# Kernel optimization log

Hardware: AMD Instinct MI355X
Metric: run time of the kernel (lower is better)

## Reference

```python
import jax, jax.numpy as jnp
import numpy as np

N = 100000   # nodes
E = 1000000  # edges
D = 128      # in_dim == out_dim (residual enabled)
EPS = 1e-5   # BatchNorm1d default eps


def setup_inputs() -> dict:
    key = jax.random.key(0)
    k = jax.random.split(key, 5)
    feature = jax.random.normal(k[0], (N, D), dtype=jnp.float32)
    src = jax.random.randint(k[1], (E,), 0, N, dtype=jnp.int32)
    dst = jax.random.randint(k[2], (E,), 0, N, dtype=jnp.int32)
    # nn.Linear(in_dim, out_dim): W is [out, in]
    W = jax.random.normal(k[3], (D, D), dtype=jnp.float32) / np.sqrt(D).astype(np.float32)
    b = jnp.zeros((D,), dtype=jnp.float32)
    gamma = jnp.ones((D,), dtype=jnp.float32)
    beta = jnp.zeros((D,), dtype=jnp.float32)
    return {"feature": feature, "src": src, "dst": dst, "W": W, "b": b,
            "gamma": gamma, "beta": beta}


def reference(feature, src, dst, W, b, gamma, beta):
    # update_all(copy_src('h'), mean): gather src features, mean-reduce onto dst
    deg = jax.ops.segment_sum(jnp.ones((E,), dtype=feature.dtype), dst,
                              num_segments=N)                      # [N]
    agg = jax.ops.segment_sum(feature[src], dst, num_segments=N)   # [N, D]
    agg = agg / jnp.maximum(deg, 1.0)[:, None]  # zero in-degree -> 0 (DGL mean)
    # NodeApplyModule: linear
    h = agg @ W.T + b                                              # [N, D]
    # BatchNorm1d over node dimension (training-mode batch stats, biased var)
    mean = jnp.mean(h, axis=0)
    var = jnp.var(h, axis=0)
    h = (h - mean) * jax.lax.rsqrt(var + EPS) * gamma + beta
    # activation, residual; dropout p=0.0 -> identity
    h = jax.nn.relu(h)
    h = feature + h
    return h
```

## Files before the change

kernel.cpp:

```cpp
#include <hip/hip_runtime.h>

typedef unsigned short u16;
typedef unsigned int u32;

#define D_DIM 128
#define CHUNK 4096
#define SCHUNK 4096
#define NPART 8

typedef __attribute__((ext_vector_type(8))) short bf16x8;
typedef __attribute__((ext_vector_type(4))) float f32x4;

__device__ __forceinline__ float bf2f(u16 h) {
    u32 u = ((u32)h) << 16;
    return __uint_as_float(u);
}
__device__ __forceinline__ u16 f2bf(float f) {
    u32 u = __float_as_uint(f);
    u32 r = (u >> 16) & 1u;
    u += 0x7fffu + r;
    return (u16)(u >> 16);
}
__device__ __forceinline__ float lo16(u32 u) { return bf2f((u16)(u & 0xffffu)); }
__device__ __forceinline__ float hi16(u32 u) { return bf2f((u16)(u >> 16)); }

__global__ void GCNLayer_76647986365164_kernel(int* p, int nwords,
                                               const u32* w, int* flag) {
    int i = blockIdx.x * blockDim.x + threadIdx.x;
    if (i < nwords) p[i] = 0;
    if (blockIdx.x == 0) {
        __shared__ int cnt;
        if (threadIdx.x == 0) cnt = 0;
        __syncthreads();
        int c = 0;
        for (int j = 0; j < 4; ++j) {
            u32 x = w[threadIdx.x * 4 + j];
            u32 e = (x >> 7) & 0xFFu;
            if (e >= 100u && e <= 140u) c++;
        }
        atomicAdd(&cnt, c);
        __syncthreads();
        if (threadIdx.x == 0) flag[0] = (cnt >= 700) ? 1 : 0;
    }
}

__global__ void k_deg(const int* __restrict__ dst, int* __restrict__ deg,
                      int* __restrict__ rank, int E) {
    int i = blockIdx.x * blockDim.x + threadIdx.x;
    if (i < E) rank[i] = atomicAdd(&deg[dst[i]], 1);
}

__global__ void k_scan_local(const int* deg, int* offs, int* bsums, int n) {
    __shared__ int tsum[256];
    const int tid = threadIdx.x;
    const int base = blockIdx.x * CHUNK + tid * 16;
    int v[16];
    int run = 0;
    for (int j = 0; j < 16; ++j) {
        int idx = base + j;
        v[j] = (idx < n) ? deg[idx] : 0;
        run += v[j];
    }
    tsum[tid] = run;
    __syncthreads();
    for (int off = 1; off < 256; off <<= 1) {
        int val = tsum[tid];
        int add = (tid >= off) ? tsum[tid - off] : 0;
        __syncthreads();
        tsum[tid] = val + add;
        __syncthreads();
    }
    int acc = tsum[tid] - run;
    for (int j = 0; j < 16; ++j) {
        int idx = base + j;
        if (idx < n) offs[idx] = acc;
        acc += v[j];
    }
    if (tid == 255) bsums[blockIdx.x] = tsum[255];
}

__global__ void k_scan_add(int* offs, const int* bsums, int n, int nblk) {
    __shared__ int carry_s;
    const int tid = threadIdx.x;
    const int b = blockIdx.x;
    if (tid == 0) {
        int c = 0;
        for (int i = 0; i < b; ++i) c += bsums[i];
        carry_s = c;
        if (b == nblk - 1) offs[n] = c + bsums[b];
    }
    __syncthreads();
    const int carry = carry_s;
    const int base = b * CHUNK + tid * 16;
    for (int j = 0; j < 16; ++j) {
        int idx = base + j;
        if (idx < n) offs[idx] += carry;
    }
}

__global__ void k_scatter(const int* __restrict__ src, const int* __restrict__ dst,
                          const int* __restrict__ rank, const int* __restrict__ offs,
                          int* __restrict__ csr, int E, int nper) {
    const int pr = blockIdx.x & (NPART - 1);
    const int s  = blockIdx.x >> 3;
    const int lo = pr * nper;
    const int hi = lo + nper;
    const int base = s * SCHUNK;
    int end = base + SCHUNK;
    if (end > E) end = E;
    for (int i = base + (int)threadIdx.x; i < end; i += 256) {
        int d = dst[i];
        if (d >= lo && d < hi) {
            csr[offs[d] + rank[i]] = src[i];
        }
    }
}

__global__ void k_aggregate(const void* feature, const int* offs,
                            const int* csr, u16* agg, const int* flag,
                            int n, int npad) {
    int node = blockIdx.x * 4 + (threadIdx.x >> 6);
    int lane = threadIdx.x & 63;
    if (node >= npad) return;
    const int g = lane >> 4;
    const int c = lane & 15;
    int bf = flag[0];
    float acc[8];
    #pragma unroll
    for (int t = 0; t < 8; ++t) acc[t] = 0.f;
    int degn = 0;
    if (node < n) {
        int s = offs[node], e = offs[node + 1];
        degn = e - s;
        if (bf) {
            const uint4* fq = (const uint4*)feature;
            for (int j = s; j < e; j += 16) {
                int j0 = j + g, j1 = j0 + 4, j2 = j0 + 8, j3 = j0 + 12;
                uint4 u0 = {0,0,0,0}, u1 = {0,0,0,0}, u2 = {0,0,0,0}, u3 = {0,0,0,0};
                if (j0 < e) u0 = fq[(size_t)csr[j0] * 16 + c];
                if (j1 < e) u1 = fq[(size_t)csr[j1] * 16 + c];
                if (j2 < e) u2 = fq[(size_t)csr[j2] * 16 + c];
                if (j3 < e) u3 = fq[(size_t)csr[j3] * 16 + c];
                #define ACC8(U) \
                    acc[0] += lo16(U.x); acc[1] += hi16(U.x); \
                    acc[2] += lo16(U.y); acc[3] += hi16(U.y); \
                    acc[4] += lo16(U.z); acc[5] += hi16(U.z); \
                    acc[6] += lo16(U.w); acc[7] += hi16(U.w);
                ACC8(u0); ACC8(u1); ACC8(u2); ACC8(u3);
                #undef ACC8
            }
        } else {
            const float4* fq = (const float4*)feature;
            for (int j = s; j < e; j += 8) {
                int j0 = j + g, j1 = j0 + 4;
                if (j0 < e) {
                    size_t b0 = (size_t)csr[j0] * 32 + c * 2;
                    float4 x = fq[b0], y = fq[b0 + 1];
                    acc[0] += x.x; acc[1] += x.y; acc[2] += x.z; acc[3] += x.w;
                    acc[4] += y.x; acc[5] += y.y; acc[6] += y.z; acc[7] += y.w;
                }
                if (j1 < e) {
                    size_t b1 = (size_t)csr[j1] * 32 + c * 2;
                    float4 x = fq[b1], y = fq[b1 + 1];
                    acc[0] += x.x; acc[1] += x.y; acc[2] += x.z; acc[3] += x.w;
                    acc[4] += y.x; acc[5] += y.y; acc[6] += y.z; acc[7] += y.w;
                }
            }
        }
    }
    #pragma unroll
    for (int t = 0; t < 8; ++t) {
        acc[t] += __shfl_xor(acc[t], 16);
        acc[t] += __shfl_xor(acc[t], 32);
    }
    float sc = 1.0f / (float)(degn > 1 ? degn : 1);
    if (g == 0) {
        uint4 o4;
        o4.x = (u32)f2bf(acc[0] * sc) | ((u32)f2bf(acc[1] * sc) << 16);
        o4.y = (u32)f2bf(acc[2] * sc) | ((u32)f2bf(acc[3] * sc) << 16);
        o4.z = (u32)f2bf(acc[4] * sc) | ((u32)f2bf(acc[5] * sc) << 16);
        o4.w = (u32)f2bf(acc[6] * sc) | ((u32)f2bf(acc[7] * sc) << 16);
        ((uint4*)(agg + (size_t)node * D_DIM))[c] = o4;
    }
}

__global__ void k_gemm(u16* agg, const void* W, const void* bias,
                       float* colsum, float* colsq, const int* flag, int n) {
    __shared__ u16 sW[128 * 136];
    __shared__ float bsum[128], bsq[128];
    const int tid = threadIdx.x;
    const int rb = blockIdx.x * 64;
    const int bf = flag[0];
    const int w = tid >> 6;
    const int lane = tid & 63;
    const int g = lane >> 4, c = lane & 15;

    if (tid < 128) { bsum[tid] = 0.f; bsq[tid] = 0.f; }

    bf16x8 afr[4];
    {
        const u16* arow = agg + (size_t)(rb + w * 16 + c) * D_DIM + g * 8;
        #pragma unroll
        for (int kt = 0; kt < 4; ++kt)
            afr[kt] = *(const bf16x8*)(arow + kt * 32);
    }

    f32x4 acc[8];
    #pragma unroll
    for (int ot = 0; ot < 8; ++ot) acc[ot] = (f32x4){0.f, 0.f, 0.f, 0.f};

    const int npass = bf ? 1 : 2;
    for (int pass = 0; pass < npass; ++pass) {
        if (bf) {
            #pragma unroll
            for (int i = 0; i < 8; ++i) {
                int e = (i * 256 + tid) * 8;
                int row = e >> 7, k = e & 127;
                *(uint4*)(&sW[row * 136 + k]) = *(const uint4*)((const u16*)W + e);
            }
        } else {
            const float* Wf = (const float*)W;
            #pragma unroll
            for (int i = 0; i < 8; ++i) {
                int e = (i * 256 + tid) * 8;
                int row = e >> 7, k = e & 127;
                float4 x = *(const float4*)(Wf + e);
                float4 y = *(const float4*)(Wf + e + 4);
                float v[8] = {x.x, x.y, x.z, x.w, y.x, y.y, y.z, y.w};
                u16 hb[8];
                #pragma unroll
                for (int j = 0; j < 8; ++j) {
                    u16 h = f2bf(v[j]);
                    if (pass == 1) h = f2bf(v[j] - bf2f(h));
                    hb[j] = h;
                }
                uint4 pk;
                pk.x = (u32)hb[0] | ((u32)hb[1] << 16);
                pk.y = (u32)hb[2] | ((u32)hb[3] << 16);
                pk.z = (u32)hb[4] | ((u32)hb[5] << 16);
                pk.w = (u32)hb[6] | ((u32)hb[7] << 16);
                *(uint4*)(&sW[row * 136 + k]) = pk;
            }
        }
        __syncthreads();
        #pragma unroll
        for (int ot = 0; ot < 8; ++ot) {
            const u16* wrow = &sW[(ot * 16 + c) * 136 + g * 8];
            #pragma unroll
            for (int kt = 0; kt < 4; ++kt) {
                bf16x8 bfr = *(const bf16x8*)(wrow + kt * 32);
                acc[ot] = __builtin_amdgcn_mfma_f32_16x16x32_bf16(
                    afr[kt], bfr, acc[ot], 0, 0, 0);
            }
        }
        if (pass + 1 < npass) __syncthreads();
    }

    const int rowbase = rb + w * 16 + g * 4;
    #pragma unroll
    for (int ot = 0; ot < 8; ++ot) {
        const int o = ot * 16 + c;
        float bv = bf ? bf2f(((const u16*)bias)[o]) : ((const float*)bias)[o];
        float s = 0.f, q = 0.f;
        float hv[4];
        #pragma unroll
        for (int r = 0; r < 4; ++r) {
            float h = acc[ot][r] + bv;
            hv[r] = h;
            if (rowbase + r < n) { s += h; q += h * h; }
        }
        #pragma unroll
        for (int r = 0; r < 4; ++r) {
            float hp = __shfl_xor(hv[r], 1);
            if (!(lane & 1)) {
                u32 pk = (u32)f2bf(hv[r]) | ((u32)f2bf(hp) << 16);
                *(u32*)(agg + (size_t)(rowbase + r) * D_DIM + o) = pk;
            }
        }
        s += __shfl_xor(s, 16); s += __shfl_xor(s, 32);
        q += __shfl_xor(q, 16); q += __shfl_xor(q, 32);
        if (g == 0) { atomicAdd(&bsum[o], s); atomicAdd(&bsq[o], q); }
    }
    __syncthreads();
    if (tid < 128) {
        atomicAdd(&colsum[tid], bsum[tid]);
        atomicAdd(&colsq[tid], bsq[tid]);
    }
}

__global__ void k_apply(const u16* h, const void* feature, const float* stats,
                        const void* gamma, const void* beta, void* outp,
                        const int* flag, int total8, float invn) {
    __shared__ float ssc[128], ssh[128];
    int tid = threadIdx.x;
    int bf = flag[0];
    if (tid < 128) {
        float mean = stats[tid] * invn;
        float var = stats[128 + tid] * invn - mean * mean;
        var = fmaxf(var, 0.f);
        float inv = rsqrtf(var + 1e-5f);
        float g = bf ? bf2f(((const u16*)gamma)[tid]) : ((const float*)gamma)[tid];
        float bb = bf ? bf2f(((const u16*)beta)[tid]) : ((const float*)beta)[tid];
        float sc = inv * g;
        ssc[tid] = sc;
        ssh[tid] = bb - mean * sc;
    }
    __syncthreads();
    int i = blockIdx.x * 256 + tid;
    if (i >= total8) return;
    size_t base = (size_t)i * 8;
    int c0 = (int)(base & (D_DIM - 1));
    uint4 h4 = ((const uint4*)h)[i];
    u32 hw[4] = {h4.x, h4.y, h4.z, h4.w};
    float hv[8];
    for (int j = 0; j < 4; ++j) { hv[2*j] = lo16(hw[j]); hv[2*j+1] = hi16(hw[j]); }
    float fv[8];
    if (bf) {
        uint4 f4 = ((const uint4*)feature)[i];
        u32 fw[4] = {f4.x, f4.y, f4.z, f4.w};
        for (int j = 0; j < 4; ++j) { fv[2*j] = lo16(fw[j]); fv[2*j+1] = hi16(fw[j]); }
    } else {
        float4 fa = ((const float4*)feature)[i * 2];
        float4 fb = ((const float4*)feature)[i * 2 + 1];
        fv[0]=fa.x; fv[1]=fa.y; fv[2]=fa.z; fv[3]=fa.w;
        fv[4]=fb.x; fv[5]=fb.y; fv[6]=fb.z; fv[7]=fb.w;
    }
    float ov[8];
    for (int j = 0; j < 8; ++j)
        ov[j] = fmaxf(hv[j] * ssc[c0 + j] + ssh[c0 + j], 0.f) + fv[j];
    if (bf) {
        uint4 o4;
        u32 ow[4];
        for (int j = 0; j < 4; ++j)
            ow[j] = (u32)f2bf(ov[2*j]) | ((u32)f2bf(ov[2*j+1]) << 16);
        o4.x = ow[0]; o4.y = ow[1]; o4.z = ow[2]; o4.w = ow[3];
        ((uint4*)outp)[i] = o4;
    } else {
        float4 oa, ob;
        oa.x=ov[0]; oa.y=ov[1]; oa.z=ov[2]; oa.w=ov[3];
        ob.x=ov[4]; ob.y=ov[5]; ob.z=ov[6]; ob.w=ov[7];
        ((float4*)outp)[i * 2] = oa;
        ((float4*)outp)[i * 2 + 1] = ob;
    }
}

static inline size_t al256s(size_t x) { return (x + 255) & ~(size_t)255; }
static inline int gmax1(int x) { return x > 0 ? x : 1; }

extern "C" void kernel_launch(void* const* d_in, const int* in_sizes, int n_in,
                              void* d_out, int out_size, void* d_ws, size_t ws_size,
                              hipStream_t stream) {
    const void* feature = d_in[0];
    const int*  src     = (const int*)d_in[1];
    const int*  dst     = (const int*)d_in[2];
    const void* W       = d_in[3];
    const void* bias    = d_in[4];
    const void* gamma   = d_in[5];
    const void* beta    = d_in[6];

    const int N = in_sizes[0] / D_DIM;
    const int E = in_sizes[1];
    const int Npad = (N + 63) & ~63;
    const int nblk = (N + CHUNK - 1) / CHUNK;
    const int nper = (N + NPART - 1) / NPART;

    char* p = (char*)d_ws;
    size_t o = 0;
    int*   flag   = (int*)(p + o);      o += 256;
    int*   deg    = (int*)(p + o);      o += (size_t)N * 4;
    float* stats  = (float*)(p + o);    o += 256 * 4;
    const int zero_words = N + 256;
    o = al256s(o);
    int*   bsums  = (int*)(p + o);      o += al256s(((size_t)nblk + 8) * 4);
    int*   offs   = (int*)(p + o);      o += al256s(((size_t)N + 8) * 4);
    int*   csr    = (int*)(p + o);      o += al256s((size_t)E * 4);
    u16*   agg    = (u16*)(p + o);      o += al256s((size_t)Npad * D_DIM * 2);
    int*   rank   = (int*)agg;
    (void)ws_size; (void)n_in; (void)out_size;

    int eb = gmax1((E + 255) / 256);
    int total8 = N * D_DIM / 8;
    int sblocks = gmax1(((E + SCHUNK - 1) / SCHUNK) * NPART);

    GCNLayer_76647986365164_kernel<<<gmax1((zero_words + 255) / 256), 256, 0, stream>>>(
        deg, zero_words, (const u32*)feature, flag);
    k_deg<<<eb, 256, 0, stream>>>(dst, deg, rank, E);
    k_scan_local<<<gmax1(nblk), 256, 0, stream>>>(deg, offs, bsums, N);
    k_scan_add<<<gmax1(nblk), 256, 0, stream>>>(offs, bsums, N, nblk);
    k_scatter<<<sblocks, 256, 0, stream>>>(src, dst, rank, offs, csr, E, nper);
    k_aggregate<<<gmax1(Npad / 4), 256, 0, stream>>>(feature, offs, csr, agg, flag, N, Npad);
    k_gemm<<<gmax1(Npad / 64), 256, 0, stream>>>(agg, W, bias, stats, stats + 128, flag, N);
    k_apply<<<gmax1((total8 + 255) / 256), 256, 0, stream>>>(
        agg, feature, stats, gamma, beta, d_out, flag, total8, 1.0f / (float)N);
}
```

Baseline: 323.8 us.

## Pre-convert fp32 features to bf16 for gather; fragment-ordered W; two-stage BN stats

After: 314.0 us. -3.0%, faster.

```diff
diff --git a/kernel.cpp b/kernel.cpp
--- a/kernel.cpp
+++ b/kernel.cpp
@@ -42,6 +42,21 @@
         __syncthreads();
         if (threadIdx.x == 0) flag[0] = (cnt >= 700) ? 1 : 0;
     }
+}
+
+__global__ void k_tobf(const float* __restrict__ f, u16* __restrict__ fb,
+                       const int* __restrict__ flag, int total8) {
+    if (flag[0]) return;
+    int i = blockIdx.x * 256 + threadIdx.x;
+    if (i >= total8) return;
+    float4 a = ((const float4*)f)[i * 2];
+    float4 b = ((const float4*)f)[i * 2 + 1];
+    uint4 o;
+    o.x = (u32)f2bf(a.x) | ((u32)f2bf(a.y) << 16);
+    o.y = (u32)f2bf(a.z) | ((u32)f2bf(a.w) << 16);
+    o.z = (u32)f2bf(b.x) | ((u32)f2bf(b.y) << 16);
+    o.w = (u32)f2bf(b.z) | ((u32)f2bf(b.w) << 16);
+    ((uint4*)fb)[i] = o;
 }
 
 __global__ void k_deg(const int* __restrict__ dst, int* __restrict__ deg,
@@ -116,15 +131,15 @@
     }
 }
 
-__global__ void k_aggregate(const void* feature, const int* offs,
-                            const int* csr, u16* agg, const int* flag,
-                            int n, int npad) {
+__global__ void k_aggregate(const void* feature, const u16* __restrict__ fcopy,
+                            const int* offs, const int* csr, u16* agg,
+                            const int* flag, int n, int npad) {
     int node = blockIdx.x * 4 + (threadIdx.x >> 6);
     int lane = threadIdx.x & 63;
     if (node >= npad) return;
     const int g = lane >> 4;
     const int c = lane & 15;
-    int bf = flag[0];
+    const u16* fb = flag[0] ? (const u16*)feature : fcopy;
     float acc[8];
     #pragma unroll
     for (int t = 0; t < 8; ++t) acc[t] = 0.f;
@@ -132,40 +147,21 @@
     if (node < n) {
         int s = offs[node], e = offs[node + 1];
         degn = e - s;
-        if (bf) {
-            const uint4* fq = (const uint4*)feature;
-            for (int j = s; j < e; j += 16) {
-                int j0 = j + g, j1 = j0 + 4, j2 = j0 + 8, j3 = j0 + 12;
-                uint4 u0 = {0,0,0,0}, u1 = {0,0,0,0}, u2 = {0,0,0,0}, u3 = {0,0,0,0};
-                if (j0 < e) u0 = fq[(size_t)csr[j0] * 16 + c];
-                if (j1 < e) u1 = fq[(size_t)csr[j1] * 16 + c];
-                if (j2 < e) u2 = fq[(size_t)csr[j2] * 16 + c];
-                if (j3 < e) u3 = fq[(size_t)csr[j3] * 16 + c];
-                #define ACC8(U) \
-                    acc[0] += lo16(U.x); acc[1] += hi16(U.x); \
-                    acc[2] += lo16(U.y); acc[3] += hi16(U.y); \
-                    acc[4] += lo16(U.z); acc[5] += hi16(U.z); \
-                    acc[6] += lo16(U.w); acc[7] += hi16(U.w);
-                ACC8(u0); ACC8(u1); ACC8(u2); ACC8(u3);
-                #undef ACC8
-            }
-        } else {
-            const float4* fq = (const float4*)feature;
-            for (int j = s; j < e; j += 8) {
-                int j0 = j + g, j1 = j0 + 4;
-                if (j0 < e) {
-                    size_t b0 = (size_t)csr[j0] * 32 + c * 2;
-                    float4 x = fq[b0], y = fq[b0 + 1];
-                    acc[0] += x.x; acc[1] += x.y; acc[2] += x.z; acc[3] += x.w;
-                    acc[4] += y.x; acc[5] += y.y; acc[6] += y.z; acc[7] += y.w;
-                }
-                if (j1 < e) {
-                    size_t b1 = (size_t)csr[j1] * 32 + c * 2;
-                    float4 x = fq[b1], y = fq[b1 + 1];
-                    acc[0] += x.x; acc[1] += x.y; acc[2] += x.z; acc[3] += x.w;
-                    acc[4] += y.x; acc[5] += y.y; acc[6] += y.z; acc[7] += y.w;
-                }
-            }
+        const uint4* fq = (const uint4*)fb;
+        for (int j = s; j < e; j += 16) {
+            int j0 = j + g, j1 = j0 + 4, j2 = j0 + 8, j3 = j0 + 12;
+            uint4 u0 = {0,0,0,0}, u1 = {0,0,0,0}, u2 = {0,0,0,0}, u3 = {0,0,0,0};
+            if (j0 < e) u0 = fq[(size_t)csr[j0] * 16 + c];
+            if (j1 < e) u1 = fq[(size_t)csr[j1] * 16 + c];
+            if (j2 < e) u2 = fq[(size_t)csr[j2] * 16 + c];
+            if (j3 < e) u3 = fq[(size_t)csr[j3] * 16 + c];
+            #define ACC8(U) \
+                acc[0] += lo16(U.x); acc[1] += hi16(U.x); \
+                acc[2] += lo16(U.y); acc[3] += hi16(U.y); \
+                acc[4] += lo16(U.z); acc[5] += hi16(U.z); \
+                acc[6] += lo16(U.w); acc[7] += hi16(U.w);
+            ACC8(u0); ACC8(u1); ACC8(u2); ACC8(u3);
+            #undef ACC8
         }
     }
     #pragma unroll
@@ -185,8 +181,8 @@
 }
 
 __global__ void k_gemm(u16* agg, const void* W, const void* bias,
-                       float* colsum, float* colsq, const int* flag, int n) {
-    __shared__ u16 sW[128 * 136];
+                       float* __restrict__ partials, const int* flag, int n) {
+    __shared__ u16 sWf[2048 * 8];
     __shared__ float bsum[128], bsq[128];
     const int tid = threadIdx.x;
     const int rb = blockIdx.x * 64;
@@ -211,21 +207,20 @@
 
     const int npass = bf ? 1 : 2;
     for (int pass = 0; pass < npass; ++pass) {
-        if (bf) {
-            #pragma unroll
-            for (int i = 0; i < 8; ++i) {
-                int e = (i * 256 + tid) * 8;
-                int row = e >> 7, k = e & 127;
-                *(uint4*)(&sW[row * 136 + k]) = *(const uint4*)((const u16*)W + e);
-            }
-        } else {
-            const float* Wf = (const float*)W;
-            #pragma unroll
-            for (int i = 0; i < 8; ++i) {
-                int e = (i * 256 + tid) * 8;
-                int row = e >> 7, k = e & 127;
-                float4 x = *(const float4*)(Wf + e);
-                float4 y = *(const float4*)(Wf + e + 4);
+        #pragma unroll
+        for (int i = 0; i < 8; ++i) {
+            int idx = i * 256 + tid;
+            int frag = idx >> 6, dl = idx & 63;
+            int ot = frag >> 2, kt = frag & 3;
+            int dg = dl >> 4, dc = dl & 15;
+            int row = ot * 16 + dc, col = kt * 32 + dg * 8;
+            if (bf) {
+                *(uint4*)(&sWf[idx * 8]) =
+                    *(const uint4*)((const u16*)W + row * 128 + col);
+            } else {
+                const float* Wf = (const float*)W;
+                float4 x = *(const float4*)(Wf + row * 128 + col);
+                float4 y = *(const float4*)(Wf + row * 128 + col + 4);
                 float v[8] = {x.x, x.y, x.z, x.w, y.x, y.y, y.z, y.w};
                 u16 hb[8];
                 #pragma unroll
@@ -239,16 +234,15 @@
                 pk.y = (u32)hb[2] | ((u32)hb[3] << 16);
                 pk.z = (u32)hb[4] | ((u32)hb[5] << 16);
                 pk.w = (u32)hb[6] | ((u32)hb[7] << 16);
-                *(uint4*)(&sW[row * 136 + k]) = pk;
+                *(uint4*)(&sWf[idx * 8]) = pk;
             }
         }
         __syncthreads();
         #pragma unroll
         for (int ot = 0; ot < 8; ++ot) {
-            const u16* wrow = &sW[(ot * 16 + c) * 136 + g * 8];
             #pragma unroll
             for (int kt = 0; kt < 4; ++kt) {
-                bf16x8 bfr = *(const bf16x8*)(wrow + kt * 32);
+                bf16x8 bfr = *(const bf16x8*)(&sWf[((ot * 4 + kt) * 64 + lane) * 8]);
                 acc[ot] = __builtin_amdgcn_mfma_f32_16x16x32_bf16(
                     afr[kt], bfr, acc[ot], 0, 0, 0);
             }
@@ -282,10 +276,17 @@
         if (g == 0) { atomicAdd(&bsum[o], s); atomicAdd(&bsq[o], q); }
     }
     __syncthreads();
-    if (tid < 128) {
-        atomicAdd(&colsum[tid], bsum[tid]);
-        atomicAdd(&colsq[tid], bsq[tid]);
-    }
+    partials[(size_t)blockIdx.x * 256 + tid] =
+        (tid < 128) ? bsum[tid] : bsq[tid - 128];
+}
+
+__global__ void k_redstats(const float* __restrict__ partials,
+                           float* __restrict__ stats, int nb) {
+    const int tid = threadIdx.x;
+    float acc = 0.f;
+    for (int r = blockIdx.x; r < nb; r += gridDim.x)
+        acc += partials[(size_t)r * 256 + tid];
+    atomicAdd(&stats[tid], acc);
 }
 
 __global__ void k_apply(const u16* h, const void* feature, const float* stats,
@@ -363,6 +364,7 @@
     const int Npad = (N + 63) & ~63;
     const int nblk = (N + CHUNK - 1) / CHUNK;
     const int nper = (N + NPART - 1) / NPART;
+    const int gb   = Npad / 64;
 
     char* p = (char*)d_ws;
     size_t o = 0;
@@ -374,8 +376,10 @@
     int*   bsums  = (int*)(p + o);      o += al256s(((size_t)nblk + 8) * 4);
     int*   offs   = (int*)(p + o);      o += al256s(((size_t)N + 8) * 4);
     int*   csr    = (int*)(p + o);      o += al256s((size_t)E * 4);
+    float* parts  = (float*)(p + o);    o += al256s((size_t)gb * 256 * 4);
     u16*   agg    = (u16*)(p + o);      o += al256s((size_t)Npad * D_DIM * 2);
     int*   rank   = (int*)agg;
+    u16*   fbf    = (u16*)d_out;
     (void)ws_size; (void)n_in; (void)out_size;
 
     int eb = gmax1((E + 255) / 256);
@@ -384,12 +388,16 @@
 
     GCNLayer_76647986365164_kernel<<<gmax1((zero_words + 255) / 256), 256, 0, stream>>>(
         deg, zero_words, (const u32*)feature, flag);
+    k_tobf<<<gmax1((total8 + 255) / 256), 256, 0, stream>>>(
+        (const float*)feature, fbf, flag, total8);
     k_deg<<<eb, 256, 0, stream>>>(dst, deg, rank, E);
     k_scan_local<<<gmax1(nblk), 256, 0, stream>>>(deg, offs, bsums, N);
     k_scan_add<<<gmax1(nblk), 256, 0, stream>>>(offs, bsums, N, nblk);
     k_scatter<<<sblocks, 256, 0, stream>>>(src, dst, rank, offs, csr, E, nper);
-    k_aggregate<<<gmax1(Npad / 4), 256, 0, stream>>>(feature, offs, csr, agg, flag, N, Npad);
-    k_gemm<<<gmax1(Npad / 64), 256, 0, stream>>>(agg, W, bias, stats, stats + 128, flag, N);
+    k_aggregate<<<gmax1(Npad / 4), 256, 0, stream>>>(
+        feature, fbf, offs, csr, agg, flag, N, Npad);
+    k_gemm<<<gmax1(gb), 256, 0, stream>>>(agg, W, bias, parts, flag, N);
+    k_redstats<<<32, 256, 0, stream>>>(parts, stats, gb);
     k_apply<<<gmax1((total8 + 255) / 256), 256, 0, stream>>>(
         agg, feature, stats, gamma, beta, d_out, flag, total8, 1.0f / (float)N);
 }
```
